# Optimization experiments

Measured on AMD Instinct MI355X. Metric: run time of the kernel, lower is better.

The kernel has to match this reference:

```python
import jax, jax.numpy as jnp
import numpy as np

B, Q, D = 4, 1024, 1024
N, DH = 16, 64  # n_head, d_head
SCALE = 1.0 / DH ** 0.5
LN_EPS = 1e-5


def setup_inputs() -> dict:
    key = jax.random.key(0)
    ks = jax.random.split(key, 10)
    return {
        "w": jax.random.normal(ks[0], (B, Q, D), jnp.float32),
        "r_emb": jax.random.normal(ks[1], (Q, N, DH), jnp.float32),
        "r_w_bias": jax.random.normal(ks[2], (N, DH), jnp.float32),
        "r_bias": jax.random.normal(ks[3], (Q, N), jnp.float32),
        # projection weights stored [in, out]; torch Linear init std = 1/sqrt(d_head)
        "Wq": jax.random.normal(ks[4], (D, N * DH), jnp.float32) * SCALE,
        "Wk": jax.random.normal(ks[5], (D, N * DH), jnp.float32) * SCALE,
        "Wv": jax.random.normal(ks[6], (D, N * DH), jnp.float32) * SCALE,
        "Wo": jax.random.normal(ks[7], (N * DH, D), jnp.float32) * SCALE,
        "ln_gamma": jnp.ones((D,), jnp.float32),
        "ln_beta": jnp.zeros((D,), jnp.float32),
    }


def _rel_shift(x):
    # x: [b, i, j, n]; pad a zero column at the end of j then drop j=0
    # equivalent to shifting left by one along j with a trailing zero.
    return jnp.concatenate([x[:, :, 1:, :], jnp.zeros_like(x[:, :, :1, :])], axis=2)


def reference(w, r_emb, r_w_bias, r_bias, Wq, Wk, Wv, Wo, ln_gamma, ln_beta):
    b, qlen, d = w.shape
    klen = qlen  # mems=None
    n, dh = r_w_bias.shape

    q_h = (w @ Wq).reshape(b, qlen, n, dh)
    k_h = (w @ Wk).reshape(b, klen, n, dh)
    v_h = (w @ Wv).reshape(b, klen, n, dh)

    rw_q = q_h + r_w_bias[None, None]                      # [b,q,n,dh]
    AC = jnp.einsum('bind,bjnd->bijn', rw_q, k_h)          # [b,q,k,n]
    B_ = jnp.einsum('bind,jnd->bijn', q_h, r_emb)          # [b,q,k,n]
    BD = _rel_shift(B_ + r_bias[None, None])               # [b,q,k,n]

    attn_score = (AC + BD) * SCALE
    attn_prob = jax.nn.softmax(attn_score, axis=2)
    attn_vec = jnp.einsum('bijn,bjnd->bind', attn_prob, v_h)
    attn_out = attn_vec.reshape(b, qlen, n * dh) @ Wo

    out = w + attn_out  # residual (post-lnorm path)
    mu = jnp.mean(out, axis=-1, keepdims=True)
    var = jnp.var(out, axis=-1, keepdims=True)
    return (out - mu) / jnp.sqrt(var + LN_EPS) * ln_gamma + ln_beta
```

## Files before the change

kernel.cpp:

```cpp
#include <hip/hip_runtime.h>
#include <hip/hip_bf16.h>

using f16 = _Float16;
typedef _Float16 f16x8 __attribute__((ext_vector_type(8)));
typedef _Float16 f16x4 __attribute__((ext_vector_type(4)));
typedef float f32x4 __attribute__((ext_vector_type(4)));

#define AS1 __attribute__((address_space(1)))
#define AS3 __attribute__((address_space(3)))

constexpr int Bc = 4, Qc = 1024, Dc = 1024, Nh = 16, DHc = 64;
constexpr int BQ = Bc * Qc;
constexpr int NHEAD = Bc * Nh;
constexpr float ATT_SCALE = 0.125f;
constexpr float LOG2E = 1.44269504088896f;

__global__ void k_f2h(const float* __restrict__ src, f16* __restrict__ dst) {
    long i8 = ((long)blockIdx.x * blockDim.x + threadIdx.x) * 8;
    float4 a = *(const float4*)&src[i8];
    float4 b = *(const float4*)&src[i8 + 4];
    f16x8 o = { (f16)a.x, (f16)a.y, (f16)a.z, (f16)a.w,
                (f16)b.x, (f16)b.y, (f16)b.z, (f16)b.w };
    *(f16x8*)&dst[i8] = o;
}

struct Ptr4 { const float* p[4]; };
__global__ void k_transpose4(Ptr4 srcs, f16* __restrict__ dst) {
    __shared__ f16 tile[32][33];
    const float* src = srcs.p[blockIdx.z];
    f16* d = dst + (long)blockIdx.z * Dc * Dc;
    int c0 = blockIdx.x * 32, r0 = blockIdx.y * 32;
#pragma unroll
    for (int dy = 0; dy < 32; dy += 8) {
        int r = r0 + threadIdx.y + dy, c = c0 + threadIdx.x;
        tile[threadIdx.y + dy][threadIdx.x] = (f16)src[(long)r * Dc + c];
    }
    __syncthreads();
#pragma unroll
    for (int dy = 0; dy < 32; dy += 8) {
        int c = c0 + threadIdx.y + dy, r = r0 + threadIdx.x;
        d[(long)c * Dc + r] = tile[threadIdx.x][threadIdx.y + dy];
    }
}

__global__ void k_fill_remb(const float* __restrict__ remb, f16* __restrict__ Ke) {
    long gid = (long)blockIdx.x * blockDim.x + threadIdx.x;
    int d8 = (int)(gid & 7) * 8;
    int j = (int)((gid >> 3) & 1023);
    int h = (int)(gid >> 13);
    int n = h & 15;
    f16x8 kv;
    if (j < 1023) {
        const float* rp = &remb[((long)(j + 1) * 16 + n) * 64 + d8];
        float4 r0 = *(const float4*)rp, r1 = *(const float4*)(rp + 4);
        kv[0] = (f16)r0.x; kv[1] = (f16)r0.y; kv[2] = (f16)r0.z; kv[3] = (f16)r0.w;
        kv[4] = (f16)r1.x; kv[5] = (f16)r1.y; kv[6] = (f16)r1.z; kv[7] = (f16)r1.w;
    } else {
        kv = f16x8{};
    }
    *(f16x8*)&Ke[(((long)h << 10) + j) * 64 + d8] = kv;
}

template <int BM, int BN, int BK, int WROWS, int WCOLS, int EPI>
__global__ __launch_bounds__(256) void k_gemm_nt(
    const f16* __restrict__ A, const f16* __restrict__ Bt, void* __restrict__ Cv,
    f16* __restrict__ qtp, f16* __restrict__ ktp, f16* __restrict__ vtp,
    int lda, int ldb, int ldc, int K)
{
    static_assert(BK == 64, "geometry below assumes BK=64");
    constexpr int TM = BM / (WROWS * 16);
    constexpr int TN = BN / (WCOLS * 16);
    __shared__ __align__(16) f16 sA[BM * 64];
    __shared__ __align__(16) f16 sB[BN * 64];

    const int tid = threadIdx.x;
    const int lane = tid & 63, wave = tid >> 6;
    const int wm = wave / WCOLS, wn = wave % WCOLS;

    const int nwg = gridDim.x * gridDim.y;
    const int flat = blockIdx.y * gridDim.x + blockIdx.x;
    const int cpx = nwg >> 3;
    const int swz = (flat & 7) * cpx + (flat >> 3);
    const int bx = swz % gridDim.x, by = swz / gridDim.x;
    const int m0 = by * BM, n0 = bx * BN;

    f32x4 acc[TM][TN] = {};

    const int lrow = lane & 15;
    const int quad = lane >> 4;
    const int srow = lane >> 3;
    const int scol = ((lane & 7) ^ (srow & 7)) * 8;

    for (int k0 = 0; k0 < K; k0 += 64) {
        __syncthreads();
        constexpr int CHA = BM / 8;
#pragma unroll
        for (int ch = 0; ch < CHA / 4; ++ch) {
            int cc = ch * 4 + wave;
            __builtin_amdgcn_global_load_lds(
                (const AS1 void*)(const void*)&A[(long)(m0 + cc * 8 + srow) * lda + k0 + scol],
                (AS3 void*)(void*)&sA[cc * 512], 16, 0, 0);
        }
        constexpr int CHB = BN / 8;
#pragma unroll
        for (int ch = 0; ch < CHB / 4; ++ch) {
            int cc = ch * 4 + wave;
            __builtin_amdgcn_global_load_lds(
                (const AS1 void*)(const void*)&Bt[(long)(n0 + cc * 8 + srow) * ldb + k0 + scol],
                (AS3 void*)(void*)&sB[cc * 512], 16, 0, 0);
        }
        __syncthreads();

#pragma unroll
        for (int kk = 0; kk < 2; ++kk) {
            const int kcb = kk * 4 + quad;
            f16x8 af[TM], bfr[TN];
#pragma unroll
            for (int mi = 0; mi < TM; ++mi) {
                int R = wm * TM * 16 + mi * 16 + lrow;
                af[mi] = *(const f16x8*)&sA[R * 64 + ((kcb ^ (lrow & 7)) * 8)];
            }
#pragma unroll
            for (int ni = 0; ni < TN; ++ni) {
                int R = wn * TN * 16 + ni * 16 + lrow;
                bfr[ni] = *(const f16x8*)&sB[R * 64 + ((kcb ^ (lrow & 7)) * 8)];
            }
#pragma unroll
            for (int mi = 0; mi < TM; ++mi)
#pragma unroll
                for (int ni = 0; ni < TN; ++ni)
                    acc[mi][ni] = __builtin_amdgcn_mfma_f32_16x16x32_f16(af[mi], bfr[ni], acc[mi][ni], 0, 0, 0);
        }
    }

    const int crow = (lane >> 4) * 4;
    const int ccol = lane & 15;
#pragma unroll
    for (int mi = 0; mi < TM; ++mi)
#pragma unroll
        for (int ni = 0; ni < TN; ++ni)
#pragma unroll
            for (int r = 0; r < 4; ++r) {
                int gm = m0 + wm * TM * 16 + mi * 16 + crow + r;
                int gn = n0 + wn * TN * 16 + ni * 16 + ccol;
                float val = acc[mi][ni][r];
                if constexpr (EPI == 0) {
                    ((f16*)Cv)[(long)gm * ldc + gn] = (f16)val;
                } else {
                    int seg = n0 >> 10;
                    int col = gn & 1023;
                    if (seg == 0) {
                        qtp[(long)gm * 1024 + col] = (f16)val;
                    } else if (seg == 1) {
                        ktp[(long)gm * 1024 + col] = (f16)val;
                    } else {
                        int b = gm >> 10, i = gm & 1023;
                        vtp[(((long)(b << 10) + col) << 10) + i] = (f16)val;
                    }
                }
            }
}

__global__ __launch_bounds__(512, 4) void k_flash(
    const f16* __restrict__ qh, const f16* __restrict__ kh,
    const f16* __restrict__ Ke, const f16* __restrict__ vT,
    const float* __restrict__ rwb, const float* __restrict__ r_bias,
    f16* __restrict__ avp)
{
    __shared__ __align__(16) f16 sKa[2][64 * 64];
    __shared__ __align__(16) f16 sKe[2][64 * 64];
    __shared__ __align__(16) f16 sVa[2][64 * 64];
    __shared__ float sRB[2][64];

    const int tid = threadIdx.x, lane = tid & 63, wave = tid >> 6;
    const int bid = blockIdx.x;
    const int h = (((bid >> 3) & 7) << 3) | (bid & 7);
    const int i0 = (bid >> 6) * 128;
    const int b = h >> 4, n = h & 15;

    const int lrow = lane & 15;
    const int quad = lane >> 4;
    const int lr3 = lane >> 3;
    const int swc = (lane & 7) ^ (lr3 & 7);

    const f16* srcK = kh + ((long)(b * Qc) + 8 * wave + lr3) * 1024 + n * 64 + swc * 8;
    const f16* srcE = Ke + ((long)h * Qc + 8 * wave + lr3) * 64 + swc * 8;
    const f16* srcV = vT + (long)h * DHc * Qc + (long)(8 * wave + lr3) * Qc + swc * 8;

    f16x8 rw0, rw1;
#pragma unroll
    for (int e = 0; e < 8; ++e) {
        rw0[e] = (f16)(rwb[n * 64 + quad * 8 + e] * ATT_SCALE);
        rw1[e] = (f16)(rwb[n * 64 + 32 + quad * 8 + e] * ATT_SCALE);
    }

    const f16 qsc = (f16)0.125f;
    f16x8 aq[4];
    {
        long rix = (long)(b * Qc + i0 + wave * 16 + lrow) * 1024 + n * 64;
        f16x8 q0 = *(const f16x8*)&qh[rix + quad * 8] * qsc;
        f16x8 q1 = *(const f16x8*)&qh[rix + 32 + quad * 8] * qsc;
        aq[0] = q0 + rw0;
        aq[1] = q1 + rw1;
        aq[2] = q0;
        aq[3] = q1;
    }

    float m_i = -1e30f, l_i = 0.0f;
    f32x4 o_acc[4] = {};

    {
        float rbv = 0.0f;
        if (tid < 64) rbv = r_bias[(tid + 1) * Nh + n] * (ATT_SCALE * LOG2E);
        __builtin_amdgcn_global_load_lds((const AS1 void*)srcK, (AS3 void*)&sKa[0][wave * 512], 16, 0, 0);
        __builtin_amdgcn_global_load_lds((const AS1 void*)srcE, (AS3 void*)&sKe[0][wave * 512], 16, 0, 0);
        __builtin_amdgcn_global_load_lds((const AS1 void*)srcV, (AS3 void*)&sVa[0][wave * 512], 16, 0, 0);
        if (tid < 64) sRB[0][tid] = rbv;
    }
    __syncthreads();

    for (int jt = 0; jt < 16; ++jt) {
        const int cur = jt & 1;

        float rbn = 0.0f;
        if (jt < 15) {
            const int j0n = (jt + 1) * 64;
            __builtin_amdgcn_global_load_lds((const AS1 void*)(srcK + (long)j0n * 1024),
                                             (AS3 void*)&sKa[cur ^ 1][wave * 512], 16, 0, 0);
            __builtin_amdgcn_global_load_lds((const AS1 void*)(srcE + (long)j0n * 64),
                                             (AS3 void*)&sKe[cur ^ 1][wave * 512], 16, 0, 0);
            __builtin_amdgcn_global_load_lds((const AS1 void*)(srcV + j0n),
                                             (AS3 void*)&sVa[cur ^ 1][wave * 512], 16, 0, 0);
            if (tid < 64) {
                int j = j0n + tid;
                rbn = (j < Qc - 1) ? r_bias[(j + 1) * Nh + n] * (ATT_SCALE * LOG2E) : 0.0f;
            }
        }

        const f16* Ka = &sKa[cur][0];
        const f16* Kb = &sKe[cur][0];
        const f16* Va = &sVa[cur][0];
        const int rsw = lrow & 7;

        f32x4 s_acc[4] = {};
#pragma unroll
        for (int ni = 0; ni < 4; ++ni) {
            int rb_ = (ni * 16 + lrow) * 64;
            f16x8 a0 = *(const f16x8*)&Ka[rb_ + ((0 + quad) ^ rsw) * 8];
            f16x8 a1 = *(const f16x8*)&Ka[rb_ + ((4 + quad) ^ rsw) * 8];
            f16x8 e0 = *(const f16x8*)&Kb[rb_ + ((0 + quad) ^ rsw) * 8];
            f16x8 e1 = *(const f16x8*)&Kb[rb_ + ((4 + quad) ^ rsw) * 8];
            s_acc[ni] = __builtin_amdgcn_mfma_f32_16x16x32_f16(a0, aq[0], s_acc[ni], 0, 0, 0);
            s_acc[ni] = __builtin_amdgcn_mfma_f32_16x16x32_f16(a1, aq[1], s_acc[ni], 0, 0, 0);
            s_acc[ni] = __builtin_amdgcn_mfma_f32_16x16x32_f16(e0, aq[2], s_acc[ni], 0, 0, 0);
            s_acc[ni] = __builtin_amdgcn_mfma_f32_16x16x32_f16(e1, aq[3], s_acc[ni], 0, 0, 0);
        }

        f16x4 pf[4];
        float mx = -1e30f;
#pragma unroll
        for (int ni = 0; ni < 4; ++ni) {
            f32x4 rb4 = *(const f32x4*)&sRB[cur][ni * 16 + quad * 4];
#pragma unroll
            for (int r = 0; r < 4; ++r) {
                float v = fmaf(s_acc[ni][r], LOG2E, rb4[r]);
                s_acc[ni][r] = v;
                mx = fmaxf(mx, v);
            }
        }
        mx = fmaxf(mx, __shfl_xor(mx, 16));
        mx = fmaxf(mx, __shfl_xor(mx, 32));
        float mn = fmaxf(m_i, mx);
        float alpha = __builtin_amdgcn_exp2f(m_i - mn);
        float sm = 0.0f;
#pragma unroll
        for (int ni = 0; ni < 4; ++ni) {
            float e0 = __builtin_amdgcn_exp2f(s_acc[ni][0] - mn);
            float e1 = __builtin_amdgcn_exp2f(s_acc[ni][1] - mn);
            float e2 = __builtin_amdgcn_exp2f(s_acc[ni][2] - mn);
            float e3 = __builtin_amdgcn_exp2f(s_acc[ni][3] - mn);
            sm += (e0 + e1) + (e2 + e3);
            f16x4 pvv; pvv[0] = (f16)e0; pvv[1] = (f16)e1; pvv[2] = (f16)e2; pvv[3] = (f16)e3;
            pf[ni] = pvv;
        }
        sm += __shfl_xor(sm, 16);
        sm += __shfl_xor(sm, 32);
        l_i = l_i * alpha + sm;
        m_i = mn;

#pragma unroll
        for (int r = 0; r < 4; ++r) {
            float al = __shfl(alpha, quad * 4 + r);
#pragma unroll
            for (int dt = 0; dt < 4; ++dt) o_acc[dt][r] *= al;
        }

#pragma unroll
        for (int nj = 0; nj < 4; ++nj) {
            int coff = ((2 * nj + (quad >> 1)) ^ rsw) * 8 + (quad & 1) * 4;
#pragma unroll
            for (int dt = 0; dt < 4; ++dt) {
                f16x4 bv = *(const f16x4*)&Va[(dt * 16 + lrow) * 64 + coff];
                o_acc[dt] = __builtin_amdgcn_mfma_f32_16x16x16f16(pf[nj], bv, o_acc[dt], 0, 0, 0);
            }
        }

        if (jt < 15) {
            if (tid < 64) sRB[cur ^ 1][tid] = rbn;
            __syncthreads();
        }
    }

    {
        float linv = 1.0f / l_i;
#pragma unroll
        for (int r = 0; r < 4; ++r) {
            float li = __shfl(linv, quad * 4 + r);
            int i = i0 + wave * 16 + quad * 4 + r;
#pragma unroll
            for (int dt = 0; dt < 4; ++dt) {
                int d = dt * 16 + lrow;
                avp[((long)(b * Qc + i) << 10) + n * 64 + d] = (f16)(o_acc[dt][r] * li);
            }
        }
    }
}

__global__ __launch_bounds__(256) void k_res_ln(const float* __restrict__ w, const f16* __restrict__ ao,
                                                const float* __restrict__ gamma, const float* __restrict__ beta,
                                                float* __restrict__ out) {
    const long base = (long)blockIdx.x * 1024;
    const int tid = threadIdx.x;
    float4 wv = *(const float4*)&w[base + tid * 4];
    f16x4 av = *(const f16x4*)&ao[base + tid * 4];
    float x[4] = { wv.x + (float)av[0], wv.y + (float)av[1],
                   wv.z + (float)av[2], wv.w + (float)av[3] };
    float s = x[0] + x[1] + x[2] + x[3];
    float s2 = x[0] * x[0] + x[1] * x[1] + x[2] * x[2] + x[3] * x[3];
#pragma unroll
    for (int off = 32; off; off >>= 1) { s += __shfl_down(s, off); s2 += __shfl_down(s2, off); }
    __shared__ float rs[4], rs2[4];
    if ((tid & 63) == 0) { rs[tid >> 6] = s; rs2[tid >> 6] = s2; }
    __syncthreads();
    s = rs[0] + rs[1] + rs[2] + rs[3];
    s2 = rs2[0] + rs2[1] + rs2[2] + rs2[3];
    float mu = s * (1.0f / 1024.0f);
    float var = s2 * (1.0f / 1024.0f) - mu * mu;
    float inv = rsqrtf(var + 1e-5f);
    float4 gv = *(const float4*)&gamma[tid * 4];
    float4 bv = *(const float4*)&beta[tid * 4];
    float4 o;
    o.x = (x[0] - mu) * inv * gv.x + bv.x;
    o.y = (x[1] - mu) * inv * gv.y + bv.y;
    o.z = (x[2] - mu) * inv * gv.z + bv.z;
    o.w = (x[3] - mu) * inv * gv.w + bv.w;
    *(float4*)&out[base + tid * 4] = o;
}

extern "C" void kernel_launch(void* const* d_in, const int* in_sizes, int n_in,
                              void* d_out, int out_size, void* d_ws, size_t ws_size,
                              hipStream_t stream) {
    const float* w_in   = (const float*)d_in[0];
    const float* r_emb  = (const float*)d_in[1];
    const float* r_wb   = (const float*)d_in[2];
    const float* r_bias = (const float*)d_in[3];
    const float* Wq     = (const float*)d_in[4];
    const float* Wk     = (const float*)d_in[5];
    const float* Wv     = (const float*)d_in[6];
    const float* Wo     = (const float*)d_in[7];
    const float* ln_g   = (const float*)d_in[8];
    const float* ln_b   = (const float*)d_in[9];
    float* out = (float*)d_out;

    char* p = (char*)d_ws;
    auto alloc = [&](size_t bytes) { char* r = p; p += (bytes + 255) & ~(size_t)255; return r; };
    f16* wh = (f16*)alloc((size_t)BQ * Dc * 2);
    f16* WT = (f16*)alloc((size_t)4 * Dc * Dc * 2);
    f16* qh = (f16*)alloc((size_t)BQ * Dc * 2);
    f16* kh = (f16*)alloc((size_t)BQ * Dc * 2);
    f16* Ke = (f16*)alloc((size_t)NHEAD * Qc * DHc * 2);
    f16* vT = (f16*)alloc((size_t)BQ * Dc * 2);
    f16* WoT = WT + (size_t)3 * Dc * Dc;
    f16* avp = wh;
    f16* ao  = Ke;

    k_f2h<<<(BQ * Dc) / (256 * 8), 256, 0, stream>>>(w_in, wh);

    Ptr4 srcs{{Wq, Wk, Wv, Wo}};
    k_transpose4<<<dim3(32, 32, 4), dim3(32, 8), 0, stream>>>(srcs, WT);

    k_fill_remb<<<(NHEAD * Qc * 8) / 256, 256, 0, stream>>>(r_emb, Ke);

    k_gemm_nt<128, 128, 64, 2, 2, 5><<<dim3(3 * Dc / 128, BQ / 128), 256, 0, stream>>>(
        wh, WT, nullptr, qh, kh, vT, Dc, Dc, 0, Dc);

    k_flash<<<512, 512, 0, stream>>>(qh, kh, Ke, vT, r_wb, r_bias, avp);

    k_gemm_nt<64, 128, 64, 2, 2, 0><<<dim3(Dc / 128, BQ / 64), 256, 0, stream>>>(
        avp, WoT, ao, nullptr, nullptr, nullptr, Dc, Dc, Dc, Dc);

    k_res_ln<<<BQ, 256, 0, stream>>>(w_in, ao, ln_g, ln_b, out);
}
```

Before: 203.4 us.

## Merge prep kernels into one launch and add lazy softmax rescaling in flash

Result: no change. 199.7 us (-1.8%).

```diff
diff --git a/kernel.cpp b/kernel.cpp
--- a/kernel.cpp
+++ b/kernel.cpp
@@ -15,50 +15,56 @@
 constexpr float ATT_SCALE = 0.125f;
 constexpr float LOG2E = 1.44269504088896f;
 
-__global__ void k_f2h(const float* __restrict__ src, f16* __restrict__ dst) {
-    long i8 = ((long)blockIdx.x * blockDim.x + threadIdx.x) * 8;
-    float4 a = *(const float4*)&src[i8];
-    float4 b = *(const float4*)&src[i8 + 4];
-    f16x8 o = { (f16)a.x, (f16)a.y, (f16)a.z, (f16)a.w,
-                (f16)b.x, (f16)b.y, (f16)b.z, (f16)b.w };
-    *(f16x8*)&dst[i8] = o;
-}
-
 struct Ptr4 { const float* p[4]; };
-__global__ void k_transpose4(Ptr4 srcs, f16* __restrict__ dst) {
-    __shared__ f16 tile[32][33];
-    const float* src = srcs.p[blockIdx.z];
-    f16* d = dst + (long)blockIdx.z * Dc * Dc;
-    int c0 = blockIdx.x * 32, r0 = blockIdx.y * 32;
-#pragma unroll
-    for (int dy = 0; dy < 32; dy += 8) {
-        int r = r0 + threadIdx.y + dy, c = c0 + threadIdx.x;
-        tile[threadIdx.y + dy][threadIdx.x] = (f16)src[(long)r * Dc + c];
-    }
-    __syncthreads();
-#pragma unroll
-    for (int dy = 0; dy < 32; dy += 8) {
-        int c = c0 + threadIdx.y + dy, r = r0 + threadIdx.x;
-        d[(long)c * Dc + r] = tile[threadIdx.x][threadIdx.y + dy];
-    }
-}
-
-__global__ void k_fill_remb(const float* __restrict__ remb, f16* __restrict__ Ke) {
-    long gid = (long)blockIdx.x * blockDim.x + threadIdx.x;
-    int d8 = (int)(gid & 7) * 8;
-    int j = (int)((gid >> 3) & 1023);
-    int h = (int)(gid >> 13);
-    int n = h & 15;
-    f16x8 kv;
-    if (j < 1023) {
-        const float* rp = &remb[((long)(j + 1) * 16 + n) * 64 + d8];
-        float4 r0 = *(const float4*)rp, r1 = *(const float4*)(rp + 4);
-        kv[0] = (f16)r0.x; kv[1] = (f16)r0.y; kv[2] = (f16)r0.z; kv[3] = (f16)r0.w;
-        kv[4] = (f16)r1.x; kv[5] = (f16)r1.y; kv[6] = (f16)r1.z; kv[7] = (f16)r1.w;
+__global__ __launch_bounds__(256) void k_prep(
+    const float* __restrict__ w_in, f16* __restrict__ wh,
+    Ptr4 srcs, f16* __restrict__ WT,
+    const float* __restrict__ remb, f16* __restrict__ Ke)
+{
+    const int bid = blockIdx.x, tid = threadIdx.x;
+    if (bid < 2048) {
+        long i8 = ((long)bid * 256 + tid) * 8;
+        float4 a = *(const float4*)&w_in[i8];
+        float4 b = *(const float4*)&w_in[i8 + 4];
+        f16x8 o = { (f16)a.x, (f16)a.y, (f16)a.z, (f16)a.w,
+                    (f16)b.x, (f16)b.y, (f16)b.z, (f16)b.w };
+        *(f16x8*)&wh[i8] = o;
+    } else if (bid < 6144) {
+        __shared__ f16 tile[32][33];
+        int idx = bid - 2048;
+        int z = idx >> 10, rem = idx & 1023;
+        int r0 = (rem >> 5) * 32, c0 = (rem & 31) * 32;
+        const float* src = srcs.p[z];
+        f16* d = WT + (long)z * Dc * Dc;
+        int tx = tid & 31, ty = tid >> 5;
+#pragma unroll
+        for (int dy = 0; dy < 32; dy += 8) {
+            int r = r0 + ty + dy, c = c0 + tx;
+            tile[ty + dy][tx] = (f16)src[(long)r * Dc + c];
+        }
+        __syncthreads();
+#pragma unroll
+        for (int dy = 0; dy < 32; dy += 8) {
+            int c = c0 + ty + dy, r = r0 + tx;
+            d[(long)c * Dc + r] = tile[tx][ty + dy];
+        }
     } else {
-        kv = f16x8{};
-    }
-    *(f16x8*)&Ke[(((long)h << 10) + j) * 64 + d8] = kv;
+        long gid = (long)(bid - 6144) * 256 + tid;
+        int d8 = (int)(gid & 7) * 8;
+        int j = (int)((gid >> 3) & 1023);
+        int h = (int)(gid >> 13);
+        int n = h & 15;
+        f16x8 kv;
+        if (j < 1023) {
+            const float* rp = &remb[((long)(j + 1) * 16 + n) * 64 + d8];
+            float4 r0 = *(const float4*)rp, r1 = *(const float4*)(rp + 4);
+            kv[0] = (f16)r0.x; kv[1] = (f16)r0.y; kv[2] = (f16)r0.z; kv[3] = (f16)r0.w;
+            kv[4] = (f16)r1.x; kv[5] = (f16)r1.y; kv[6] = (f16)r1.z; kv[7] = (f16)r1.w;
+        } else {
+            kv = f16x8{};
+        }
+        *(f16x8*)&Ke[(((long)h << 10) + j) * 64 + d8] = kv;
+    }
 }
 
 template <int BM, int BN, int BK, int WROWS, int WCOLS, int EPI>
@@ -257,43 +263,49 @@
         }
 
         f16x4 pf[4];
-        float mx = -1e30f;
+        float mx = -1e30f, sm = 0.0f;
 #pragma unroll
         for (int ni = 0; ni < 4; ++ni) {
             f32x4 rb4 = *(const f32x4*)&sRB[cur][ni * 16 + quad * 4];
+            f16x4 pvv;
 #pragma unroll
             for (int r = 0; r < 4; ++r) {
                 float v = fmaf(s_acc[ni][r], LOG2E, rb4[r]);
                 s_acc[ni][r] = v;
                 mx = fmaxf(mx, v);
-            }
-        }
-        mx = fmaxf(mx, __shfl_xor(mx, 16));
-        mx = fmaxf(mx, __shfl_xor(mx, 32));
-        float mn = fmaxf(m_i, mx);
-        float alpha = __builtin_amdgcn_exp2f(m_i - mn);
-        float sm = 0.0f;
-#pragma unroll
-        for (int ni = 0; ni < 4; ++ni) {
-            float e0 = __builtin_amdgcn_exp2f(s_acc[ni][0] - mn);
-            float e1 = __builtin_amdgcn_exp2f(s_acc[ni][1] - mn);
-            float e2 = __builtin_amdgcn_exp2f(s_acc[ni][2] - mn);
-            float e3 = __builtin_amdgcn_exp2f(s_acc[ni][3] - mn);
-            sm += (e0 + e1) + (e2 + e3);
-            f16x4 pvv; pvv[0] = (f16)e0; pvv[1] = (f16)e1; pvv[2] = (f16)e2; pvv[3] = (f16)e3;
+                float e = __builtin_amdgcn_exp2f(v - m_i);
+                sm += e;
+                pvv[r] = (f16)e;
+            }
             pf[ni] = pvv;
         }
-        sm += __shfl_xor(sm, 16);
-        sm += __shfl_xor(sm, 32);
-        l_i = l_i * alpha + sm;
-        m_i = mn;
-
-#pragma unroll
-        for (int r = 0; r < 4; ++r) {
-            float al = __shfl(alpha, quad * 4 + r);
-#pragma unroll
-            for (int dt = 0; dt < 4; ++dt) o_acc[dt][r] *= al;
-        }
+        if (!__all(mx - m_i <= 8.0f)) {
+            float wmx = fmaxf(mx, __shfl_xor(mx, 16));
+            wmx = fmaxf(wmx, __shfl_xor(wmx, 32));
+            float mn = fmaxf(m_i, wmx);
+            float alpha = __builtin_amdgcn_exp2f(m_i - mn);
+            sm = 0.0f;
+#pragma unroll
+            for (int ni = 0; ni < 4; ++ni) {
+                f16x4 pvv;
+#pragma unroll
+                for (int r = 0; r < 4; ++r) {
+                    float e = __builtin_amdgcn_exp2f(s_acc[ni][r] - mn);
+                    sm += e;
+                    pvv[r] = (f16)e;
+                }
+                pf[ni] = pvv;
+            }
+            l_i *= alpha;
+#pragma unroll
+            for (int r = 0; r < 4; ++r) {
+                float al = __shfl(alpha, quad * 4 + r);
+#pragma unroll
+                for (int dt = 0; dt < 4; ++dt) o_acc[dt][r] *= al;
+            }
+            m_i = mn;
+        }
+        l_i += sm;
 
 #pragma unroll
         for (int nj = 0; nj < 4; ++nj) {
@@ -311,6 +323,8 @@
         }
     }
 
+    l_i += __shfl_xor(l_i, 16);
+    l_i += __shfl_xor(l_i, 32);
     {
         float linv = 1.0f / l_i;
 #pragma unroll
@@ -384,12 +398,8 @@
     f16* avp = wh;
     f16* ao  = Ke;
 
-    k_f2h<<<(BQ * Dc) / (256 * 8), 256, 0, stream>>>(w_in, wh);
-
     Ptr4 srcs{{Wq, Wk, Wv, Wo}};
-    k_transpose4<<<dim3(32, 32, 4), dim3(32, 8), 0, stream>>>(srcs, WT);
-
-    k_fill_remb<<<(NHEAD * Qc * 8) / 256, 256, 0, stream>>>(r_emb, Ke);
+    k_prep<<<8192, 256, 0, stream>>>(w_in, wh, srcs, WT, r_emb, Ke);
 
     k_gemm_nt<128, 128, 64, 2, 2, 5><<<dim3(3 * Dc / 128, BQ / 128), 256, 0, stream>>>(
         wh, WT, nullptr, qh, kh, vT, Dc, Dc, 0, Dc);
```
